# Kernel optimization log

Hardware: AMD Instinct MI355X
Metric: run time of the kernel (lower is better)

The kernel has to match this reference:

```python
import jax, jax.numpy as jnp
import numpy as np
import math

N_HEADS = 16
D_MODEL = 1024
D_K = D_MODEL // N_HEADS


def setup_inputs() -> dict:
    key = jax.random.key(0)
    ks = jax.random.split(key, 11)
    B, S = 4, 2048
    scale = 1.0 / math.sqrt(D_MODEL)
    return {
        "q": jax.random.normal(ks[0], (B, S, D_MODEL), jnp.float32),
        "k": jax.random.normal(ks[1], (B, S, D_MODEL), jnp.float32),
        "v": jax.random.normal(ks[2], (B, S, D_MODEL), jnp.float32),
        "Wq": jax.random.normal(ks[3], (D_MODEL, D_MODEL), jnp.float32) * scale,
        "bq": jax.random.normal(ks[4], (D_MODEL,), jnp.float32) * 0.01,
        "Wk": jax.random.normal(ks[5], (D_MODEL, D_MODEL), jnp.float32) * scale,
        "bk": jax.random.normal(ks[6], (D_MODEL,), jnp.float32) * 0.01,
        "Wv": jax.random.normal(ks[7], (D_MODEL, D_MODEL), jnp.float32) * scale,
        "bv": jax.random.normal(ks[8], (D_MODEL,), jnp.float32) * 0.01,
        "Wo": jax.random.normal(ks[9], (D_MODEL, D_MODEL), jnp.float32) * scale,
        "bo": jax.random.normal(ks[10], (D_MODEL,), jnp.float32) * 0.01,
    }


def reference(q, k, v, Wq, bq, Wk, bk, Wv, bv, Wo, bo):
    B, S, _ = q.shape
    # linear projections, then split heads: [B, H, S, d_k]
    def proj(x, W, b):
        y = x @ W.T + b
        return y.reshape(B, -1, N_HEADS, D_K).transpose(0, 2, 1, 3)
    qh = proj(q, Wq, bq)
    kh = proj(k, Wk, bk)
    vh = proj(v, Wv, bv)
    # scaled dot-product attention (mask=None, dropout p=0 -> identity)
    scores = jnp.einsum("bhqd,bhkd->bhqk", qh, kh) / math.sqrt(D_K)
    attn = jax.nn.softmax(scores, axis=-1)
    out = jnp.einsum("bhqk,bhkd->bhqd", attn, vh)  # [B, H, S, d_k]
    concat = out.transpose(0, 2, 1, 3).reshape(B, -1, D_MODEL)
    return concat @ Wo.T + bo
```

## Files before the change

### kernel.cpp

```cpp
#include <hip/hip_runtime.h>
#include <stdint.h>

#define DEVI __device__ __forceinline__

typedef __attribute__((ext_vector_type(8))) short bf16x8;
typedef __attribute__((ext_vector_type(4))) float f32x4;
typedef __attribute__((ext_vector_type(4))) int int4v;

DEVI unsigned short f2bf(float f) {
  union { float f; unsigned u; } v; v.f = f;
  return (unsigned short)((v.u + 0x7FFFu + ((v.u >> 16) & 1u)) >> 16);
}

__global__ __launch_bounds__(256) void cvt_kernel(const float* __restrict__ s,
                                                  unsigned short* __restrict__ d, int n) {
  int i = (blockIdx.x * 256 + threadIdx.x) * 4;
  if (i >= n) return;
  float4 v = *(const float4*)(s + i);
  union { unsigned short u[4]; uint2 w; } o;
  o.u[0] = f2bf(v.x); o.u[1] = f2bf(v.y); o.u[2] = f2bf(v.z); o.u[3] = f2bf(v.w);
  *(uint2*)(d + i) = o.w;
}

template<bool A_F32, int OUT_MODE>
__global__ __launch_bounds__(256) void gemm_bt(const void* __restrict__ Aptr,
                                               const unsigned short* __restrict__ Bmat,
                                               const float* __restrict__ bias,
                                               void* __restrict__ Cptr, float oscale) {
  constexpr int K = 1024;
  constexpr int LDT = 72;
  __shared__ __align__(16) unsigned short Alds[128][LDT];
  __shared__ __align__(16) unsigned short Blds[128][LDT];
  const int tid = threadIdx.x;
  const int lane = tid & 63, w = tid >> 6;
  const int wm = w >> 1, wn = w & 1;
  const int l15 = lane & 15, lq = lane >> 4;
  const int rowBase = blockIdx.x * 128, colBase = blockIdx.y * 128;
  const int arow = tid >> 1, acol = (tid & 1) * 32;

  f32x4 acc[4][4] = {};

  float4 afp[8]; int4v abf[4]; int4v bbf[4];
  auto loadA = [&](int k0) {
    if (A_F32) {
      const float* p = (const float*)Aptr + (size_t)(rowBase + arow) * K + k0 + acol;
#pragma unroll
      for (int i = 0; i < 8; i++) afp[i] = *(const float4*)(p + i * 4);
    } else {
      const unsigned short* p = (const unsigned short*)Aptr + (size_t)(rowBase + arow) * K + k0 + acol;
#pragma unroll
      for (int i = 0; i < 4; i++) abf[i] = *(const int4v*)(p + i * 8);
    }
  };
  auto loadB = [&](int k0) {
    const unsigned short* p = Bmat + (size_t)(colBase + arow) * K + k0 + acol;
#pragma unroll
    for (int i = 0; i < 4; i++) bbf[i] = *(const int4v*)(p + i * 8);
  };

  loadA(0); loadB(0);

  for (int k0 = 0; k0 < K; k0 += 64) {
    __syncthreads();
    if (A_F32) {
      unsigned short t[32];
#pragma unroll
      for (int i = 0; i < 8; i++) {
        t[i*4+0] = f2bf(afp[i].x); t[i*4+1] = f2bf(afp[i].y);
        t[i*4+2] = f2bf(afp[i].z); t[i*4+3] = f2bf(afp[i].w);
      }
#pragma unroll
      for (int i = 0; i < 4; i++) *(int4v*)&Alds[arow][acol + i*8] = *(const int4v*)&t[i*8];
    } else {
#pragma unroll
      for (int i = 0; i < 4; i++) *(int4v*)&Alds[arow][acol + i*8] = abf[i];
    }
#pragma unroll
    for (int i = 0; i < 4; i++) *(int4v*)&Blds[arow][acol + i*8] = bbf[i];
    if (k0 + 64 < K) { loadA(k0 + 64); loadB(k0 + 64); }
    __syncthreads();
#pragma unroll
    for (int kc = 0; kc < 2; kc++) {
      bf16x8 af[4], bfr[4];
#pragma unroll
      for (int m = 0; m < 4; m++)
        af[m] = *(const bf16x8*)&Alds[wm*64 + m*16 + l15][kc*32 + lq*8];
#pragma unroll
      for (int n = 0; n < 4; n++)
        bfr[n] = *(const bf16x8*)&Blds[wn*64 + n*16 + l15][kc*32 + lq*8];
#pragma unroll
      for (int m = 0; m < 4; m++)
#pragma unroll
        for (int n = 0; n < 4; n++)
          acc[m][n] = __builtin_amdgcn_mfma_f32_16x16x32_bf16(af[m], bfr[n], acc[m][n], 0, 0, 0);
    }
  }
#pragma unroll
  for (int n = 0; n < 4; n++) {
    int col = colBase + wn*64 + n*16 + l15;
    float bv = bias[col];
#pragma unroll
    for (int m = 0; m < 4; m++) {
      int row0 = rowBase + wm*64 + m*16 + lq*4;
#pragma unroll
      for (int r = 0; r < 4; r++) {
        int row = row0 + r;
        float val = (acc[m][n][r] + bv) * oscale;
        if (OUT_MODE == 0) {
          ((float*)Cptr)[(size_t)row * 1024 + col] = val;
        } else {
          unsigned short* C = (unsigned short*)Cptr;
          int hh = col >> 6, dd = col & 63;
          int bb = row >> 11, ss = row & 2047;
          int bh = bb * 16 + hh;
          if (OUT_MODE == 1) C[(((size_t)bh * 2048 + ss) << 6) + dd] = f2bf(val);
          else               C[((size_t)bh << 17) + ((size_t)dd << 11) + ss] = f2bf(val);
        }
      }
    }
  }
}

__global__ __launch_bounds__(256, 2) void attn_kernel(const unsigned short* __restrict__ Qh,
                                                      const unsigned short* __restrict__ Kh,
                                                      const unsigned short* __restrict__ VT,
                                                      unsigned short* __restrict__ Ob) {
  const int tid = threadIdx.x, lane = tid & 63, w = tid >> 6;
  const int l15 = lane & 15, lq = lane >> 4;
  const int bid = blockIdx.x;
  const int xcd = bid & 7, slot = bid >> 3;
  const int bh = xcd * 8 + (slot >> 4), qt = slot & 15;
  const int qbase = qt * 128 + w * 32;
  const unsigned short* Qp = Qh + ((size_t)bh << 17);
  const unsigned short* Kp = Kh + ((size_t)bh << 17);
  const unsigned short* Vp = VT + ((size_t)bh << 17);

  bf16x8 qb[2][2];
#pragma unroll
  for (int mi = 0; mi < 2; mi++)
#pragma unroll
    for (int kc = 0; kc < 2; kc++)
      qb[mi][kc] = *(const bf16x8*)(Qp + (size_t)(qbase + mi*16 + l15) * 64 + kc*32 + lq*8);

  f32x4 oacc[2][4] = {};
  float mrun[2] = {-1e30f, -1e30f};
  float lrun[2] = {0.f, 0.f};

  bf16x8 kaA[4][2], kaB[4][2];
  auto loadK = [&](bf16x8 (&ka)[4][2], int kt) {
#pragma unroll
    for (int kb = 0; kb < 4; kb++)
#pragma unroll
      for (int kc = 0; kc < 2; kc++)
        ka[kb][kc] = *(const bf16x8*)(Kp + (size_t)(kt + kb*16 + l15) * 64 + kc*32 + lq*8);
  };
  loadK(kaA, 0);

  auto tile = [&](bf16x8 (&ka)[4][2], bf16x8 (&kan)[4][2], int kt, int ktn) {
    bf16x8 va[4][2];
#pragma unroll
    for (int db = 0; db < 4; db++)
#pragma unroll
      for (int win = 0; win < 2; win++)
        va[db][win] = *(const bf16x8*)(Vp + (size_t)(db*16 + l15) * 2048 + kt + win*32 + lq*8);

    f32x4 sf[2][4] = {};
#pragma unroll
    for (int kc = 0; kc < 2; kc++)
#pragma unroll
      for (int mi = 0; mi < 2; mi++)
#pragma unroll
        for (int kb = 0; kb < 4; kb++)
          sf[mi][kb] = __builtin_amdgcn_mfma_f32_16x16x32_bf16(ka[kb][kc], qb[mi][kc], sf[mi][kb], 0, 0, 0);

    if (ktn < 2048) loadK(kan, ktn);

    float pm[2];
#pragma unroll
    for (int mi = 0; mi < 2; mi++) {
      float t0 = fmaxf(fmaxf(sf[mi][0][0], sf[mi][0][1]), fmaxf(sf[mi][0][2], sf[mi][0][3]));
      float t1 = fmaxf(fmaxf(sf[mi][1][0], sf[mi][1][1]), fmaxf(sf[mi][1][2], sf[mi][1][3]));
      float t2 = fmaxf(fmaxf(sf[mi][2][0], sf[mi][2][1]), fmaxf(sf[mi][2][2], sf[mi][2][3]));
      float t3 = fmaxf(fmaxf(sf[mi][3][0], sf[mi][3][1]), fmaxf(sf[mi][3][2], sf[mi][3][3]));
      float t = fmaxf(fmaxf(t0, t1), fmaxf(t2, t3));
      t = fmaxf(t, __shfl_xor(t, 16));
      t = fmaxf(t, __shfl_xor(t, 32));
      pm[mi] = t;
    }
    if (__any((pm[0] > mrun[0] + 11.5f) || (pm[1] > mrun[1] + 11.5f))) {
#pragma unroll
      for (int mi = 0; mi < 2; mi++) {
        float mnew = fmaxf(mrun[mi], pm[mi]);
        float alpha = __builtin_amdgcn_exp2f(mrun[mi] - mnew);
        mrun[mi] = mnew; lrun[mi] *= alpha;
#pragma unroll
        for (int db = 0; db < 4; db++)
#pragma unroll
          for (int r = 0; r < 4; r++) oacc[mi][db][r] *= alpha;
      }
    }
#pragma unroll
    for (int mi = 0; mi < 2; mi++) {
      float s = 0.f;
#pragma unroll
      for (int kb = 0; kb < 4; kb++)
#pragma unroll
        for (int r = 0; r < 4; r++) {
          float e = __builtin_amdgcn_exp2f(sf[mi][kb][r] - mrun[mi]);
          sf[mi][kb][r] = e; s += e;
        }
      s += __shfl_xor(s, 16);
      s += __shfl_xor(s, 32);
      lrun[mi] += s;
    }

    const int half = lq >> 1;
    const unsigned selp = (unsigned)((lq ^ half) & 1);
#pragma unroll
    for (int mi = 0; mi < 2; mi++) {
      bf16x8 pb[2];
#pragma unroll
      for (int win = 0; win < 2; win++) {
        unsigned u00, u01, u10, u11;
        asm("v_cvt_pk_bf16_f32 %0, %1, %2" : "=v"(u00) : "v"(sf[mi][2*win][0]),   "v"(sf[mi][2*win][1]));
        asm("v_cvt_pk_bf16_f32 %0, %1, %2" : "=v"(u01) : "v"(sf[mi][2*win][2]),   "v"(sf[mi][2*win][3]));
        asm("v_cvt_pk_bf16_f32 %0, %1, %2" : "=v"(u10) : "v"(sf[mi][2*win+1][0]), "v"(sf[mi][2*win+1][1]));
        asm("v_cvt_pk_bf16_f32 %0, %1, %2" : "=v"(u11) : "v"(sf[mi][2*win+1][2]), "v"(sf[mi][2*win+1][3]));
        unsigned lw0 = half ? u10 : u00, lw1 = half ? u11 : u01;
        unsigned sa0 = half ? u00 : u10, sa1 = half ? u01 : u11;
        unsigned y0 = (unsigned)__shfl_xor((int)sa0, 32);
        unsigned y1 = (unsigned)__shfl_xor((int)sa1, 32);
        unsigned z0 = selp ? lw0 : y0, z1 = selp ? lw1 : y1;
        unsigned r0 = (unsigned)__shfl_xor((int)z0, 16);
        unsigned r1 = (unsigned)__shfl_xor((int)z1, 16);
        unsigned wl0 = (lq == 0) ? lw0 : ((lq == 2) ? y0 : r0);
        unsigned wl1 = (lq == 0) ? lw1 : ((lq == 2) ? y1 : r1);
        unsigned wh0 = (lq == 3) ? lw0 : ((lq == 1) ? y0 : r0);
        unsigned wh1 = (lq == 3) ? lw1 : ((lq == 1) ? y1 : r1);
        union { unsigned u[4]; bf16x8 v; } pf;
        pf.u[0] = wl0; pf.u[1] = wl1; pf.u[2] = wh0; pf.u[3] = wh1;
        pb[win] = pf.v;
      }
#pragma unroll
      for (int db = 0; db < 4; db++) {
        oacc[mi][db] = __builtin_amdgcn_mfma_f32_16x16x32_bf16(va[db][0], pb[0], oacc[mi][db], 0, 0, 0);
        oacc[mi][db] = __builtin_amdgcn_mfma_f32_16x16x32_bf16(va[db][1], pb[1], oacc[mi][db], 0, 0, 0);
      }
    }
  };

  for (int kt = 0; kt < 2048; kt += 128) {
    tile(kaA, kaB, kt, kt + 64);
    tile(kaB, kaA, kt + 64, kt + 128);
  }

  const int b = bh >> 4, h = bh & 15;
#pragma unroll
  for (int mi = 0; mi < 2; mi++) {
    const float inv = 1.0f / lrun[mi];
    const int q = qbase + mi*16 + l15;
    const size_t base = ((size_t)b * 2048 + q) * 1024 + h * 64;
#pragma unroll
    for (int db = 0; db < 4; db++) {
      float e0 = oacc[mi][db][0] * inv, e1 = oacc[mi][db][1] * inv;
      float e2 = oacc[mi][db][2] * inv, e3 = oacc[mi][db][3] * inv;
      unsigned w0, w1;
      asm("v_cvt_pk_bf16_f32 %0, %1, %2" : "=v"(w0) : "v"(e0), "v"(e1));
      asm("v_cvt_pk_bf16_f32 %0, %1, %2" : "=v"(w1) : "v"(e2), "v"(e3));
      uint2 st; st.x = w0; st.y = w1;
      *(uint2*)(Ob + base + db*16 + lq*4) = st;
    }
  }
}

extern "C" void kernel_launch(void* const* d_in, const int* in_sizes, int n_in,
                              void* d_out, int out_size, void* d_ws, size_t ws_size,
                              hipStream_t stream) {
  const float* q  = (const float*)d_in[0];
  const float* k  = (const float*)d_in[1];
  const float* v  = (const float*)d_in[2];
  const float* Wq = (const float*)d_in[3];
  const float* bq = (const float*)d_in[4];
  const float* Wk = (const float*)d_in[5];
  const float* bk = (const float*)d_in[6];
  const float* Wv = (const float*)d_in[7];
  const float* bv = (const float*)d_in[8];
  const float* Wo = (const float*)d_in[9];
  const float* bo = (const float*)d_in[10];

  unsigned short* Wqb = (unsigned short*)d_ws;
  unsigned short* Wkb = Wqb + 1024 * 1024;
  unsigned short* Wvb = Wkb + 1024 * 1024;
  unsigned short* Wob = Wvb + 1024 * 1024;
  unsigned short* Ob  = Wob + 1024 * 1024;
  unsigned short* Qh  = Ob + (size_t)8192 * 1024;
  unsigned short* Kh  = Qh + (size_t)8192 * 1024;
  unsigned short* VT  = Kh + (size_t)8192 * 1024;

  const float QSCALE = 0.125f * 1.44269504f;

  cvt_kernel<<<1024, 256, 0, stream>>>(Wq, Wqb, 1024 * 1024);
  cvt_kernel<<<1024, 256, 0, stream>>>(Wk, Wkb, 1024 * 1024);
  cvt_kernel<<<1024, 256, 0, stream>>>(Wv, Wvb, 1024 * 1024);
  cvt_kernel<<<1024, 256, 0, stream>>>(Wo, Wob, 1024 * 1024);

  dim3 g(64, 8), blk(256);
  gemm_bt<true, 1><<<g, blk, 0, stream>>>(q, Wqb, bq, Qh, QSCALE);
  gemm_bt<true, 1><<<g, blk, 0, stream>>>(k, Wkb, bk, Kh, 1.0f);
  gemm_bt<true, 2><<<g, blk, 0, stream>>>(v, Wvb, bv, VT, 1.0f);

  attn_kernel<<<dim3(1024), blk, 0, stream>>>(Qh, Kh, VT, Ob);

  gemm_bt<false, 0><<<g, blk, 0, stream>>>(Ob, Wob, bo, (float*)d_out, 1.0f);
}
```

Measured before the change: 545.8 us.

## Load GEMM B tiles via direct global-to-LDS and split attention into single-wave blocks

In the projection GEMMs the B (weight) tile now goes straight from global memory into an unpadded LDS buffer using global_load_lds, replacing the register-staged prefetch. This saves registers and VGPR traffic, but drops the software prefetch overlap for B and the padding that avoided LDS bank conflicts. The attention kernel is relaunched as 4096 one-wave blocks instead of 1024 four-wave blocks, which gives the scheduler finer granularity. Each wave now loads its K/V tiles independently, so any sharing of those tiles across waves in a block is lost.

```diff
diff --git a/kernel.cpp b/kernel.cpp
--- a/kernel.cpp
+++ b/kernel.cpp
@@ -10,6 +10,11 @@
 DEVI unsigned short f2bf(float f) {
   union { float f; unsigned u; } v; v.f = f;
   return (unsigned short)((v.u + 0x7FFFu + ((v.u >> 16) & 1u)) >> 16);
+}
+
+DEVI void gll16(const void* g, void* l) {
+  __builtin_amdgcn_global_load_lds((__attribute__((address_space(1))) void*)g,
+                                   (__attribute__((address_space(3))) void*)l, 16, 0, 0);
 }
 
 __global__ __launch_bounds__(256) void cvt_kernel(const float* __restrict__ s,
@@ -30,7 +35,7 @@
   constexpr int K = 1024;
   constexpr int LDT = 72;
   __shared__ __align__(16) unsigned short Alds[128][LDT];
-  __shared__ __align__(16) unsigned short Blds[128][LDT];
+  __shared__ __align__(16) unsigned short Bl[128][64];
   const int tid = threadIdx.x;
   const int lane = tid & 63, w = tid >> 6;
   const int wm = w >> 1, wn = w & 1;
@@ -40,7 +45,7 @@
 
   f32x4 acc[4][4] = {};
 
-  float4 afp[8]; int4v abf[4]; int4v bbf[4];
+  float4 afp[8]; int4v abf[4];
   auto loadA = [&](int k0) {
     if (A_F32) {
       const float* p = (const float*)Aptr + (size_t)(rowBase + arow) * K + k0 + acol;
@@ -52,16 +57,15 @@
       for (int i = 0; i < 4; i++) abf[i] = *(const int4v*)(p + i * 8);
     }
   };
-  auto loadB = [&](int k0) {
-    const unsigned short* p = Bmat + (size_t)(colBase + arow) * K + k0 + acol;
-#pragma unroll
-    for (int i = 0; i < 4; i++) bbf[i] = *(const int4v*)(p + i * 8);
-  };
-
-  loadA(0); loadB(0);
+  loadA(0);
 
   for (int k0 = 0; k0 < K; k0 += 64) {
     __syncthreads();
+#pragma unroll
+    for (int i = 0; i < 4; i++) {
+      int r = w * 32 + i * 8 + (lane >> 3);
+      gll16(Bmat + (size_t)(colBase + r) * 1024 + k0 + (lane & 7) * 8, &Bl[w * 32 + i * 8][0]);
+    }
     if (A_F32) {
       unsigned short t[32];
 #pragma unroll
@@ -75,9 +79,7 @@
 #pragma unroll
       for (int i = 0; i < 4; i++) *(int4v*)&Alds[arow][acol + i*8] = abf[i];
     }
-#pragma unroll
-    for (int i = 0; i < 4; i++) *(int4v*)&Blds[arow][acol + i*8] = bbf[i];
-    if (k0 + 64 < K) { loadA(k0 + 64); loadB(k0 + 64); }
+    if (k0 + 64 < K) loadA(k0 + 64);
     __syncthreads();
 #pragma unroll
     for (int kc = 0; kc < 2; kc++) {
@@ -87,7 +89,7 @@
         af[m] = *(const bf16x8*)&Alds[wm*64 + m*16 + l15][kc*32 + lq*8];
 #pragma unroll
       for (int n = 0; n < 4; n++)
-        bfr[n] = *(const bf16x8*)&Blds[wn*64 + n*16 + l15][kc*32 + lq*8];
+        bfr[n] = *(const bf16x8*)&Bl[wn*64 + n*16 + l15][kc*32 + lq*8];
 #pragma unroll
       for (int m = 0; m < 4; m++)
 #pragma unroll
@@ -121,16 +123,16 @@
   }
 }
 
-__global__ __launch_bounds__(256, 2) void attn_kernel(const unsigned short* __restrict__ Qh,
-                                                      const unsigned short* __restrict__ Kh,
-                                                      const unsigned short* __restrict__ VT,
-                                                      unsigned short* __restrict__ Ob) {
-  const int tid = threadIdx.x, lane = tid & 63, w = tid >> 6;
+__global__ __launch_bounds__(64, 4) void attn_kernel(const unsigned short* __restrict__ Qh,
+                                                     const unsigned short* __restrict__ Kh,
+                                                     const unsigned short* __restrict__ VT,
+                                                     unsigned short* __restrict__ Ob) {
+  const int lane = threadIdx.x & 63;
   const int l15 = lane & 15, lq = lane >> 4;
   const int bid = blockIdx.x;
   const int xcd = bid & 7, slot = bid >> 3;
-  const int bh = xcd * 8 + (slot >> 4), qt = slot & 15;
-  const int qbase = qt * 128 + w * 32;
+  const int bh = xcd * 8 + (slot >> 6), qs = slot & 63;
+  const int qbase = qs * 32;
   const unsigned short* Qp = Qh + ((size_t)bh << 17);
   const unsigned short* Kp = Kh + ((size_t)bh << 17);
   const unsigned short* Vp = VT + ((size_t)bh << 17);
@@ -309,7 +311,7 @@
   gemm_bt<true, 1><<<g, blk, 0, stream>>>(k, Wkb, bk, Kh, 1.0f);
   gemm_bt<true, 2><<<g, blk, 0, stream>>>(v, Wvb, bv, VT, 1.0f);
 
-  attn_kernel<<<dim3(1024), blk, 0, stream>>>(Qh, Kh, VT, Ob);
+  attn_kernel<<<dim3(4096), dim3(64), 0, stream>>>(Qh, Kh, VT, Ob);
 
   gemm_bt<false, 0><<<g, blk, 0, stream>>>(Ob, Wob, bo, (float*)d_out, 1.0f);
 }
```

After: 746.0 us. +36.7%, slower.
